# Performance work log

Measured on AMD Instinct MI355X. Metric: run time of the kernel, lower is better.

## Reference

```python
import jax, jax.numpy as jnp
import numpy as np

B, S, D, H, HD = 2, 2048, 1024, 16, 64
K, L = 1024, 4  # num_codes, vq_levels


def setup_inputs() -> dict:
    key = jax.random.key(0)
    ks = jax.random.split(key, 12)
    w = lambda k, shape: jax.random.normal(k, shape, jnp.float32) * 0.02
    return {
        "x": jax.random.normal(ks[0], (B, S, D), jnp.float32),
        "ln1_g": jnp.ones((D,), jnp.float32), "ln1_b": jnp.zeros((D,), jnp.float32),
        "wq": w(ks[1], (D, D)), "wk": w(ks[2], (D, D)), "wv": w(ks[3], (D, D)),
        "wg": w(ks[4], (D, D)), "wo": w(ks[5], (D, D)),
        "ln2_g": jnp.ones((D,), jnp.float32), "ln2_b": jnp.zeros((D,), jnp.float32),
        "w1": w(ks[6], (D, 4 * D)), "b1": jnp.zeros((4 * D,), jnp.float32),
        "w2": w(ks[7], (4 * D, D)), "b2": jnp.zeros((D,), jnp.float32),
        "ln3_g": jnp.ones((D,), jnp.float32), "ln3_b": jnp.zeros((D,), jnp.float32),
        "codebooks": jax.random.uniform(ks[8], (L, K, D), jnp.float32, -1.0 / K, 1.0 / K),
    }


def _ln(x, g, b):
    m = jnp.mean(x, -1, keepdims=True)
    v = jnp.var(x, -1, keepdims=True)
    return (x - m) / jnp.sqrt(v + 1e-5) * g + b


def _rope(x):  # x: [B, S, H, HD]
    hd = x.shape[-1]
    inv = 1.0 / (10000.0 ** (jnp.arange(0, hd, 2, dtype=jnp.float32) / hd))
    t = jnp.arange(x.shape[1], dtype=jnp.float32)
    f = jnp.einsum('i,j->ij', t, inv)               # [S, HD/2]
    emb = jnp.concatenate([f, f], -1)               # [S, HD]
    cos = jnp.cos(emb)[None, :, None, :]
    sin = jnp.sin(emb)[None, :, None, :]
    x1, x2 = jnp.split(x, 2, -1)
    rot = jnp.concatenate([-x2, x1], -1)
    return x * cos + rot * sin


def reference(x, ln1_g, ln1_b, wq, wk, wv, wg, wo, ln2_g, ln2_b,
              w1, b1, w2, b2, ln3_g, ln3_b, codebooks):
    # --- retention sub-block (pre-LN) ---
    h = _ln(x, ln1_g, ln1_b)
    q = (h @ wq).reshape(B, S, H, HD)
    k = (h @ wk).reshape(B, S, H, HD)
    v = (h @ wv).reshape(B, S, H, HD)
    q, k = _rope(q), _rope(k)
    q, k, v = (a.transpose(0, 2, 1, 3) for a in (q, k, v))  # [B,H,S,HD]
    i = jnp.arange(S)
    dmask = jnp.tril(i[:, None] - i[None, :]).astype(jnp.float32)  # [S,S], >=0
    gamma = (1.0 - jnp.exp2(-5.0 - jnp.arange(H, dtype=jnp.float32)))[:, None, None]
    decay = (gamma ** dmask) * jnp.tril(jnp.ones((S, S), jnp.float32))  # [H,S,S]
    ret = jnp.einsum('bhqd,bhkd->bhqk', q, k) / np.sqrt(HD).astype(np.float32) * decay
    o = jnp.einsum('bhqk,bhkd->bhqd', ret, v).transpose(0, 2, 1, 3).reshape(B, S, D)
    g = jax.nn.silu(h @ wg)
    x = x + (o * g) @ wo
    # --- MLP sub-block (pre-LN) ---
    h2 = _ln(x, ln2_g, ln2_b)
    x = x + (jax.nn.gelu(h2 @ w1 + b1, approximate=False) @ w2 + b2)
    # --- residual vector quantizer ---
    xn = _ln(x, ln3_g, ln3_b)
    residual, total = xn, jnp.zeros_like(xn)
    ql, el = 0.0, 0.0
    for lvl in range(L):
        cb = codebooks[lvl]                         # [K, D]
        flat = residual.reshape(-1, D)              # [B*S, D]
        d2 = (jnp.sum(flat ** 2, 1, keepdims=True)
              + jnp.sum(cb ** 2, 1) - 2.0 * flat @ cb.T)
        idx = jnp.argmin(d2, 1)
        quant = cb[idx].reshape(xn.shape)
        ql = ql + jnp.mean((quant - jax.lax.stop_gradient(residual)) ** 2)
        el = el + jnp.mean((jax.lax.stop_gradient(quant) - residual) ** 2)
        total = total + quant
        residual = residual - jax.lax.stop_gradient(quant)
    final = xn + jax.lax.stop_gradient(total - xn)  # straight-through
    return (x + final, ql / L, el / L)
```

## Files before the change

kernel.cpp:

```cpp
#include <hip/hip_runtime.h>
#include <cstdint>
#include <cstddef>

#define DEV __device__ __forceinline__

typedef __attribute__((ext_vector_type(8))) short bf16x8;
typedef __attribute__((ext_vector_type(4))) float f32x4;

typedef const __attribute__((address_space(1))) void gl_void;
typedef __attribute__((address_space(3))) void lds_void;

DEV unsigned short f2bf(float f){
  union { float f; uint32_t u; } v; v.f = f;
  uint32_t r = v.u + 0x7FFFu + ((v.u >> 16) & 1u);
  return (unsigned short)(r >> 16);
}
DEV float bf2f(unsigned short u){
  union { uint32_t u; float f; } v; v.u = ((uint32_t)u) << 16; return v.f;
}
DEV uint32_t packbf2(float a, float b){
  return (uint32_t)f2bf(a) | ((uint32_t)f2bf(b) << 16);
}

__global__ void ln_kernel(const float* __restrict__ x, const float* __restrict__ gw,
                          const float* __restrict__ bw, unsigned short* __restrict__ obf,
                          float* __restrict__ of32)
{
  const int row = blockIdx.x, t = threadIdx.x;
  const float4 v = ((const float4*)(x + (size_t)row*1024))[t];
  float s  = v.x + v.y + v.z + v.w;
  float s2 = v.x*v.x + v.y*v.y + v.z*v.z + v.w*v.w;
  #pragma unroll
  for (int o = 32; o >= 1; o >>= 1){ s += __shfl_down(s, o); s2 += __shfl_down(s2, o); }
  __shared__ float red[8];
  const int w = t >> 6, ln = t & 63;
  if (ln == 0){ red[w] = s; red[4+w] = s2; }
  __syncthreads();
  const float fs  = red[0]+red[1]+red[2]+red[3];
  const float fs2 = red[4]+red[5]+red[6]+red[7];
  const float mean = fs * (1.0f/1024.0f);
  const float var  = fs2 * (1.0f/1024.0f) - mean*mean;
  const float rstd = rsqrtf(var + 1e-5f);
  const float4 gv = ((const float4*)gw)[t];
  const float4 bv = ((const float4*)bw)[t];
  float4 o4;
  o4.x = (v.x-mean)*rstd*gv.x + bv.x;
  o4.y = (v.y-mean)*rstd*gv.y + bv.y;
  o4.z = (v.z-mean)*rstd*gv.z + bv.z;
  o4.w = (v.w-mean)*rstd*gv.w + bv.w;
  if (of32) ((float4*)(of32 + (size_t)row*1024))[t] = o4;
  ushort4 ob; ob.x = f2bf(o4.x); ob.y = f2bf(o4.y); ob.z = f2bf(o4.z); ob.w = f2bf(o4.w);
  ((ushort4*)(obf + (size_t)row*1024))[t] = ob;
}

struct Ptr5 { const float* p[5]; };
__global__ void transpose_cvt5(Ptr5 in, unsigned short* __restrict__ out)
{
  __shared__ float tile[32][33];
  const float* src = in.p[blockIdx.z];
  unsigned short* dst = out + (size_t)blockIdx.z*1048576;
  const int c0 = blockIdx.x*32, r0 = blockIdx.y*32;
  const int tx = threadIdx.x & 31, ty = threadIdx.x >> 5;
  #pragma unroll
  for (int i = 0; i < 32; i += 8)
    tile[ty+i][tx] = src[(size_t)(r0+ty+i)*1024 + c0 + tx];
  __syncthreads();
  #pragma unroll
  for (int i = 0; i < 32; i += 8)
    dst[(size_t)(c0+ty+i)*1024 + r0 + tx] = f2bf(tile[tx][ty+i]);
}

__global__ void transpose_cvt(const float* __restrict__ in, unsigned short* __restrict__ out,
                              int R, int C)
{
  __shared__ float tile[32][33];
  const int c0 = blockIdx.x*32, r0 = blockIdx.y*32;
  const int tx = threadIdx.x & 31, ty = threadIdx.x >> 5;
  #pragma unroll
  for (int i = 0; i < 32; i += 8)
    tile[ty+i][tx] = in[(size_t)(r0+ty+i)*C + c0 + tx];
  __syncthreads();
  #pragma unroll
  for (int i = 0; i < 32; i += 8)
    out[(size_t)(c0+ty+i)*R + r0 + tx] = f2bf(tile[tx][ty+i]);
}

__global__ void cvtnorm_kernel(const float* __restrict__ cb, unsigned short* __restrict__ cbbf,
                               float* __restrict__ cbn2)
{
  const int code = blockIdx.x, t = threadIdx.x;
  const float4 v = ((const float4*)(cb + (size_t)code*1024))[t];
  ushort4 o; o.x = f2bf(v.x); o.y = f2bf(v.y); o.z = f2bf(v.z); o.w = f2bf(v.w);
  ((ushort4*)(cbbf + (size_t)code*1024))[t] = o;
  float s = v.x*v.x + v.y*v.y + v.z*v.z + v.w*v.w;
  #pragma unroll
  for (int off = 32; off >= 1; off >>= 1) s += __shfl_down(s, off);
  __shared__ float red[4];
  if ((t & 63) == 0) red[t >> 6] = s;
  __syncthreads();
  if (t == 0) cbn2[code] = red[0]+red[1]+red[2]+red[3];
}

__global__ void rope_tab(float2* __restrict__ rt)
{
  const int i = blockIdx.x*256 + threadIdx.x;
  const int s = i >> 5, j = i & 31;
  const float ang = (float)s * exp2f(-(float)j * 0.4152410118609203f);
  float sn, cs; sincosf(ang, &sn, &cs);
  rt[i] = make_float2(cs, sn);
}

template<int EPI>
__global__ __launch_bounds__(512, 2) void gemm256(
    const unsigned short* __restrict__ A, const unsigned short* __restrict__ BT,
    unsigned short* __restrict__ C, const float* __restrict__ bias,
    const float2* __restrict__ rt, int M, int N, int K)
{
  __shared__ __align__(16) unsigned short SH[49152];
  const int t = threadIdx.x;
  const int w = t >> 6, ln = t & 63, lg = ln >> 4, lc = ln & 15;
  const int wm = w >> 2, wn = w & 3;
  const int gx = gridDim.x, nwg = gridDim.x * gridDim.y;
  int lin = blockIdx.y * gx + blockIdx.x;
  lin = (lin >> 3) + (lin & 7) * (nwg >> 3);
  const int m0 = (lin / gx) * 256, n0 = (lin % gx) * 256;
  const int nkt = K >> 5;

  f32x4 acc[8][4] = {};

  auto stage = [&](int buf, int kt){
    #pragma unroll
    for (int isB = 0; isB < 2; ++isB){
      const unsigned short* src = isB ? BT : A;
      const int mb = isB ? n0 : m0;
      #pragma unroll
      for (int j = 0; j < 2; ++j){
        const int u = j*512 + t;
        const int ro = u >> 2;
        const int su = (u & 3) ^ ((ro >> 1) & 3);
        __builtin_amdgcn_global_load_lds(
          (gl_void*)(src + (size_t)(mb + ro)*K + (size_t)kt*32 + su*8),
          (lds_void*)&SH[buf*16384 + isB*8192 + (j*512 + (t & ~63))*8],
          16, 0, 0);
      }
    }
  };

  auto ldA = [&](int buf, int mf) -> bf16x8 {
    const int R = wm*128 + mf*16 + lc;
    const int cu = lg ^ ((R >> 1) & 3);
    return *(const bf16x8*)&SH[buf*16384 + (R*4 + cu)*8];
  };
  auto ldB = [&](int buf, int nf) -> bf16x8 {
    const int R = wn*64 + nf*16 + lc;
    const int cu = lg ^ ((R >> 1) & 3);
    return *(const bf16x8*)&SH[buf*16384 + 8192 + (R*4 + cu)*8];
  };

  stage(0, 0); stage(1, 1);
  asm volatile("s_waitcnt vmcnt(4)" ::: "memory");
  __builtin_amdgcn_s_barrier();

  for (int kt = 0; kt < nkt; ++kt){
    const int cur = kt % 3;
    const bool pf = (kt + 2 < nkt);
    bf16x8 aF[4], bF[4];

    if (pf) stage((kt + 2) % 3, kt + 2);
    #pragma unroll
    for (int f = 0; f < 4; ++f){ aF[f] = ldA(cur, f); bF[f] = ldB(cur, f); }
    __builtin_amdgcn_s_barrier();
    __builtin_amdgcn_s_setprio(1);
    #pragma unroll
    for (int mf = 0; mf < 4; ++mf)
      #pragma unroll
      for (int nf = 0; nf < 4; ++nf)
        acc[mf][nf] = __builtin_amdgcn_mfma_f32_16x16x32_bf16(aF[mf], bF[nf], acc[mf][nf], 0, 0, 0);
    __builtin_amdgcn_s_setprio(0);
    asm volatile("s_waitcnt lgkmcnt(0)" ::: "memory");
    __builtin_amdgcn_s_barrier();

    #pragma unroll
    for (int f = 0; f < 4; ++f) aF[f] = ldA(cur, 4 + f);
    __builtin_amdgcn_s_barrier();
    __builtin_amdgcn_s_setprio(1);
    #pragma unroll
    for (int mf = 0; mf < 4; ++mf)
      #pragma unroll
      for (int nf = 0; nf < 4; ++nf)
        acc[4+mf][nf] = __builtin_amdgcn_mfma_f32_16x16x32_bf16(aF[mf], bF[nf], acc[4+mf][nf], 0, 0, 0);
    __builtin_amdgcn_s_setprio(0);
    asm volatile("s_waitcnt lgkmcnt(0)" ::: "memory");
    if (pf) asm volatile("s_waitcnt vmcnt(4)" ::: "memory");
    else    asm volatile("s_waitcnt vmcnt(0)" ::: "memory");
    __builtin_amdgcn_s_barrier();
  }

  const int mrow = m0 + wm*128, ncol = n0 + wn*64;
  if constexpr (EPI == 3){
    const int sect = ncol >> 10;
    unsigned short* outp = C + (size_t)sect*4194304;
    #pragma unroll
    for (int mf = 0; mf < 8; ++mf){
      #pragma unroll
      for (int r = 0; r < 4; ++r){
        const int row = mrow + mf*16 + lg*4 + r;
        const int s_ = row & 2047;
        #pragma unroll
        for (int nf = 0; nf < 4; ++nf){
          const int c1 = (ncol + nf*16 + lc) & 1023;
          float v = acc[mf][nf][r];
          if (sect <= 1){
            const float2 cs = rt[(s_ << 5) + (c1 & 31)];
            const float vp = acc[mf][nf ^ 2][r];
            v = (c1 & 32) ? (v*cs.x + vp*cs.y) : (v*cs.x - vp*cs.y);
          } else if (sect == 3){
            v = v * (1.0f / (1.0f + __expf(-v)));
          }
          outp[(size_t)row*1024 + c1] = f2bf(v);
        }
      }
    }
  } else {
    #pragma unroll
    for (int mf = 0; mf < 8; ++mf){
      #pragma unroll
      for (int r = 0; r < 4; ++r){
        const int row = mrow + mf*16 + lg*4 + r;
        #pragma unroll
        for (int nf = 0; nf < 4; ++nf){
          const int col = ncol + nf*16 + lc;
          float v = acc[mf][nf][r] + bias[col];
          v = 0.5f * v * (1.0f + erff(v * 0.70710678118654752f));
          C[(size_t)row*N + col] = f2bf(v);
        }
      }
    }
  }
}

template<int EPI, bool BIAS, bool RES, bool OUTBF, int NSPLIT>
__global__ __launch_bounds__(256, 2) void gemm64_bt(
    const unsigned short* __restrict__ A, const unsigned short* __restrict__ BT,
    void* __restrict__ Cv, const float* __restrict__ bias, const float* __restrict__ resid,
    int M, int N, int K)
{
  __shared__ __align__(16) unsigned short As[3][64*64];
  __shared__ __align__(16) unsigned short Bs[3][128*64];
  const int t = threadIdx.x;
  const int w = t >> 6, ln = t & 63, lg = ln >> 4, lc = ln & 15;
  const int gx = gridDim.x, nwg = gridDim.x * gridDim.y;
  int lin = blockIdx.y * gx + blockIdx.x;
  lin = (lin >> 3) + (lin & 7) * (nwg >> 3);
  const int bx = lin % gx, by = lin / gx;
  const int m0 = by * 64, n0 = bx * 128;
  const int wr = (w >> 1) * 32, wc = (w & 1) * 64;
  f32x4 acc[2][4] = {};
  const int nkt = (K >> 6) / NSPLIT;
  const int ktb = (NSPLIT > 1) ? blockIdx.z * nkt : 0;

  auto stage = [&](int buf, int kt){
    #pragma unroll
    for (int c = 0; c < 2; ++c){
      const int chunk = c*256 + t;
      const int row = chunk >> 3;
      const int kb = (((chunk & 7) << 4) ^ ((row & 7) << 4)) >> 1;
      __builtin_amdgcn_global_load_lds(
          (gl_void*)(A + (size_t)(m0+row)*K + (size_t)(ktb+kt)*64 + kb),
          (lds_void*)&As[buf][(c*256 + w*64)*8], 16, 0, 0);
    }
    #pragma unroll
    for (int c = 0; c < 4; ++c){
      const int chunk = c*256 + t;
      const int row = chunk >> 3;
      const int kb = (((chunk & 7) << 4) ^ ((row & 7) << 4)) >> 1;
      __builtin_amdgcn_global_load_lds(
          (gl_void*)(BT + (size_t)(n0+row)*K + (size_t)(ktb+kt)*64 + kb),
          (lds_void*)&Bs[buf][(c*256 + w*64)*8], 16, 0, 0);
    }
  };

  stage(0, 0); stage(1, 1);
  asm volatile("s_waitcnt vmcnt(6)" ::: "memory");
  __builtin_amdgcn_s_barrier();

  for (int kt = 0; kt < nkt; ++kt){
    const int cur = kt % 3;
    const bool pf = (kt + 2 < nkt);
    if (pf) stage((kt + 2) % 3, kt + 2);
    __builtin_amdgcn_s_setprio(1);
    #pragma unroll
    for (int ks = 0; ks < 2; ++ks){
      bf16x8 af[2], bfr[4];
      #pragma unroll
      for (int i = 0; i < 2; ++i){
        const int rowA = wr + i*16 + lc;
        const int colA = (((ks<<6) + (lg<<4)) ^ ((rowA & 7) << 4)) >> 1;
        af[i] = *(const bf16x8*)&As[cur][rowA*64 + colA];
      }
      #pragma unroll
      for (int i = 0; i < 4; ++i){
        const int rowB = wc + i*16 + lc;
        const int colB = (((ks<<6) + (lg<<4)) ^ ((rowB & 7) << 4)) >> 1;
        bfr[i] = *(const bf16x8*)&Bs[cur][rowB*64 + colB];
      }
      #pragma unroll
      for (int m = 0; m < 2; ++m)
        #pragma unroll
        for (int n = 0; n < 4; ++n)
          acc[m][n] = __builtin_amdgcn_mfma_f32_16x16x32_bf16(af[m], bfr[n], acc[m][n], 0, 0, 0);
    }
    __builtin_amdgcn_s_setprio(0);
    asm volatile("s_waitcnt lgkmcnt(0)" ::: "memory");
    if (pf) asm volatile("s_waitcnt vmcnt(6)" ::: "memory");
    else    asm volatile("s_waitcnt vmcnt(0)" ::: "memory");
    __builtin_amdgcn_s_barrier();
  }

  if constexpr (EPI == 4){
    #pragma unroll
    for (int m = 0; m < 2; ++m){
      #pragma unroll
      for (int r = 0; r < 4; ++r){
        float best = 3.4e38f; int bi = 0;
        #pragma unroll
        for (int n = 0; n < 4; ++n){
          const int col = n0 + wc + n*16 + lc;
          const float d = bias[col] - 2.0f*acc[m][n][r];
          if (d < best){ best = d; bi = col; }
        }
        #pragma unroll
        for (int o = 1; o < 16; o <<= 1){
          const float ob = __shfl_xor(best, o);
          const int oi = __shfl_xor(bi, o);
          if (ob < best || (ob == best && oi < bi)){ best = ob; bi = oi; }
        }
        if (lc == 0){
          const int row = m0 + wr + m*16 + lg*4 + r;
          ((float2*)Cv)[row*16 + bx*2 + (w & 1)] = make_float2(best, (float)bi);
        }
      }
    }
    return;
  }

  float* Cp = (float*)Cv + (NSPLIT > 1 ? (size_t)blockIdx.z * (size_t)M * N : 0);
  #pragma unroll
  for (int m = 0; m < 2; ++m){
    #pragma unroll
    for (int n = 0; n < 4; ++n){
      #pragma unroll
      for (int r = 0; r < 4; ++r){
        const int row = m0 + wr + m*16 + lg*4 + r;
        const int col = n0 + wc + n*16 + lc;
        float v = acc[m][n][r];
        if constexpr (BIAS) v += bias[col];
        if constexpr (RES) v += resid[(size_t)row*N + col];
        if constexpr (OUTBF) ((unsigned short*)Cv)[(size_t)row*N + col] = f2bf(v);
        else                 Cp[(size_t)row*N + col] = v;
      }
    }
  }
}

__global__ void splitk_reduce(const float* __restrict__ p, const float* __restrict__ bias,
                              const float* __restrict__ resid, float* __restrict__ out)
{
  const int i = blockIdx.x*256 + threadIdx.x;
  const float4 a = ((const float4*)p)[i];
  const float4 b = ((const float4*)(p + 4194304))[i];
  const float4 rv = ((const float4*)resid)[i];
  const float4 bv = ((const float4*)bias)[i & 255];
  float4 o;
  o.x = a.x + b.x + rv.x + bv.x;
  o.y = a.y + b.y + rv.y + bv.y;
  o.z = a.z + b.z + rv.z + bv.z;
  o.w = a.w + b.w + rv.w + bv.w;
  ((float4*)out)[i] = o;
}

__global__ __launch_bounds__(256, 2) void chunk_sum(
    const unsigned short* __restrict__ kb, const unsigned short* __restrict__ vb,
    float* __restrict__ Tbuf)
{
  __shared__ unsigned short KT[64*72];
  __shared__ unsigned short VT[64*72];
  const int t = threadIdx.x, w = t >> 6, ln = t & 63, lg = ln >> 4, lc = ln & 15;
  const int blk = blockIdx.x;
  const int bh = blk >> 5, c = blk & 31;
  const int b = bh >> 4, hh = bh & 15;
  const float lg2g = log2f(1.0f - exp2f(-5.0f - (float)hh));
  #pragma unroll
  for (int ch = 0; ch < 2; ++ch){
    const int chunk = ch*256 + t;
    const int i = chunk >> 3, d0 = (chunk & 7)*8;
    const size_t gofs = ((size_t)(b*2048 + c*64 + i))*1024 + hh*64 + d0;
    const float wi = exp2f(lg2g * (float)(64 - i));
    union {uint4 u; unsigned short s[8];} kv, vv;
    kv.u = *(const uint4*)(kb + gofs);
    vv.u = *(const uint4*)(vb + gofs);
    #pragma unroll
    for (int j = 0; j < 8; ++j){
      KT[(d0+j)*72 + i] = f2bf(bf2f(kv.s[j]) * wi);
      VT[(d0+j)*72 + i] = vv.s[j];
    }
  }
  __syncthreads();
  f32x4 acc[4] = {};
  #pragma unroll
  for (int ks = 0; ks < 2; ++ks){
    const bf16x8 af = *(const bf16x8*)&KT[(w*16 + lc)*72 + ks*32 + lg*8];
    #pragma unroll
    for (int n = 0; n < 4; ++n){
      const bf16x8 bf = *(const bf16x8*)&VT[(n*16 + lc)*72 + ks*32 + lg*8];
      acc[n] = __builtin_amdgcn_mfma_f32_16x16x32_bf16(af, bf, acc[n], 0, 0, 0);
    }
  }
  float* out = Tbuf + (size_t)blk*4096;
  #pragma unroll
  for (int n = 0; n < 4; ++n)
    #pragma unroll
    for (int r = 0; r < 4; ++r)
      out[(w*16 + lg*4 + r)*64 + n*16 + lc] = acc[n][r];
}

__global__ void chunk_scan(const float* __restrict__ Tbuf, unsigned short* __restrict__ statesT)
{
  const int bh = blockIdx.x, t = threadIdx.x;
  const int hh = bh & 15;
  const float gamma = 1.0f - exp2f(-5.0f - (float)hh);
  const float g64 = exp2f(log2f(gamma) * 64.0f);
  float S[16];
  #pragma unroll
  for (int j = 0; j < 16; ++j) S[j] = 0.f;
  const int dv = t >> 2, d0 = (t & 3) * 16;
  for (int c = 0; c < 32; ++c){
    const size_t base = ((size_t)(bh*32 + c))*4096;
    union { unsigned short s[8]; uint4 u; } p0, p1;
    #pragma unroll
    for (int j = 0; j < 8; ++j){ p0.s[j] = f2bf(S[j]); p1.s[j] = f2bf(S[8+j]); }
    *(uint4*)(statesT + base + t*16)     = p0.u;
    *(uint4*)(statesT + base + t*16 + 8) = p1.u;
    #pragma unroll
    for (int j = 0; j < 16; ++j)
      S[j] = g64*S[j] + Tbuf[base + (size_t)(d0 + j)*64 + dv];
  }
}

__global__ __launch_bounds__(256, 2) void retention_chunk(
    const unsigned short* __restrict__ qb, const unsigned short* __restrict__ kb,
    const unsigned short* __restrict__ vb, const unsigned short* __restrict__ gb,
    const unsigned short* __restrict__ statesT, unsigned short* __restrict__ og)
{
  __shared__ unsigned short VT[64*72];
  __shared__ unsigned short Pw[64*72];
  const int t = threadIdx.x, w = t >> 6, ln = t & 63, lg = ln >> 4, lc = ln & 15;
  const int blk = blockIdx.x;
  const int bh = blk >> 5, c = blk & 31;
  const int b = bh >> 4, hh = bh & 15;
  const float lg2g = log2f(1.0f - exp2f(-5.0f - (float)hh));
  float gpr[4];
  #pragma unroll
  for (int r = 0; r < 4; ++r) gpr[r] = exp2f(-lg2g * (float)r);
  const size_t rowbase = (size_t)(b*2048 + c*64);

  #pragma unroll
  for (int ch = 0; ch < 2; ++ch){
    const int chunk = ch*256 + t;
    const int i = chunk >> 3, d0 = (chunk & 7)*8;
    union {uint4 u; unsigned short s[8];} vv;
    vv.u = *(const uint4*)(vb + (rowbase + i)*1024 + hh*64 + d0);
    #pragma unroll
    for (int j = 0; j < 8; ++j) VT[(d0+j)*72 + i] = vv.s[j];
  }

  bf16x8 Qf[2], Kf[4][2];
  #pragma unroll
  for (int ks = 0; ks < 2; ++ks){
    union {uint4 u; bf16x8 f;} cv;
    cv.u = *(const uint4*)(qb + (rowbase + w*16 + lc)*1024 + hh*64 + ks*32 + lg*8);
    Qf[ks] = cv.f;
    #pragma unroll
    for (int mt = 0; mt < 4; ++mt){
      union {uint4 u; bf16x8 f;} kv;
      kv.u = *(const uint4*)(kb + (rowbase + mt*16 + lc)*1024 + hh*64 + ks*32 + lg*8);
      Kf[mt][ks] = kv.f;
    }
  }

  f32x4 st[4] = {};
  #pragma unroll
  for (int ks = 0; ks < 2; ++ks)
    #pragma unroll
    for (int mt = 0; mt < 4; ++mt)
      st[mt] = __builtin_amdgcn_mfma_f32_16x16x32_bf16(Kf[mt][ks], Qf[ks], st[mt], 0, 0, 0);

  __syncthreads();

  #pragma unroll
  for (int mt = 0; mt < 4; ++mt){
    const int kp = mt*16 + lg*4;
    const int qrow = w*16 + lc;
    const int delta0 = qrow - kp;
    const float dec0 = exp2f(lg2g * (float)delta0) * 0.125f;
    float vals[4];
    #pragma unroll
    for (int r = 0; r < 4; ++r)
      vals[r] = (delta0 >= r) ? st[mt][r] * dec0 * gpr[r] : 0.0f;
    uint2 pk; pk.x = packbf2(vals[0], vals[1]); pk.y = packbf2(vals[2], vals[3]);
    *(uint2*)&Pw[qrow*72 + kp] = pk;
  }

  f32x4 acc[4] = {};
  const unsigned short* Sbase = statesT + (size_t)blk*4096;
  #pragma unroll
  for (int ks = 0; ks < 2; ++ks)
    #pragma unroll
    for (int n = 0; n < 4; ++n){
      union {uint4 u; bf16x8 f;} sv;
      sv.u = *(const uint4*)(Sbase + (n*16 + lc)*64 + ks*32 + lg*8);
      acc[n] = __builtin_amdgcn_mfma_f32_16x16x32_bf16(Qf[ks], sv.f, acc[n], 0, 0, 0);
    }
  #pragma unroll
  for (int n = 0; n < 4; ++n)
    #pragma unroll
    for (int r = 0; r < 4; ++r)
      acc[n][r] *= exp2f(lg2g * (float)(w*16 + lg*4 + r)) * 0.125f;

  #pragma unroll
  for (int ks = 0; ks < 2; ++ks){
    const bf16x8 Pf = *(const bf16x8*)&Pw[(w*16 + lc)*72 + ks*32 + lg*8];
    #pragma unroll
    for (int n = 0; n < 4; ++n){
      const bf16x8 Vf = *(const bf16x8*)&VT[(n*16 + lc)*72 + ks*32 + lg*8];
      acc[n] = __builtin_amdgcn_mfma_f32_16x16x32_bf16(Pf, Vf, acc[n], 0, 0, 0);
    }
  }

  #pragma unroll
  for (int n = 0; n < 4; ++n){
    #pragma unroll
    for (int r = 0; r < 4; ++r){
      const size_t row = rowbase + w*16 + lg*4 + r;
      const int col = hh*64 + n*16 + lc;
      const float gv = bf2f(gb[row*1024 + col]);
      og[row*1024 + col] = f2bf(acc[n][r] * gv);
    }
  }
}

__global__ void rvq_update3(const float* __restrict__ cb_l, const float2* __restrict__ partials,
                            const float* __restrict__ res_in, float* __restrict__ res_out,
                            unsigned short* __restrict__ resb, float* __restrict__ qlpart, int lvl)
{
  const int m = blockIdx.x, t = threadIdx.x;
  __shared__ int sid;
  if (t == 0){
    float best = 3.4e38f; int bi = 0;
    #pragma unroll
    for (int p = 0; p < 16; ++p){
      const float2 pr = partials[m*16 + p];
      if (pr.x < best){ best = pr.x; bi = (int)pr.y; }
    }
    sid = bi;
  }
  __syncthreads();
  const int id = sid;
  const float4 qv = ((const float4*)(cb_l + (size_t)id*1024))[t];
  const float4 rv = ((const float4*)(res_in + (size_t)m*1024))[t];
  float4 nr; nr.x = rv.x - qv.x; nr.y = rv.y - qv.y; nr.z = rv.z - qv.z; nr.w = rv.w - qv.w;
  ((float4*)(res_out + (size_t)m*1024))[t] = nr;
  ushort4 nb; nb.x = f2bf(nr.x); nb.y = f2bf(nr.y); nb.z = f2bf(nr.z); nb.w = f2bf(nr.w);
  ((ushort4*)(resb + (size_t)m*1024))[t] = nb;
  float s = nr.x*nr.x + nr.y*nr.y + nr.z*nr.z + nr.w*nr.w;
  #pragma unroll
  for (int o = 32; o >= 1; o >>= 1) s += __shfl_down(s, o);
  __shared__ float red[4];
  if ((t & 63) == 0) red[t >> 6] = s;
  __syncthreads();
  if (t == 0) qlpart[lvl*4096 + m] = red[0]+red[1]+red[2]+red[3];
}

__global__ void final_add3(const float* __restrict__ x2, const float* __restrict__ xn,
                           const float* __restrict__ res4, float* __restrict__ out)
{
  const int i = blockIdx.x*256 + threadIdx.x;
  const float4 a = ((const float4*)x2)[i];
  const float4 b = ((const float4*)xn)[i];
  const float4 c = ((const float4*)res4)[i];
  float4 o;
  o.x = a.x + b.x - c.x;
  o.y = a.y + b.y - c.y;
  o.z = a.z + b.z - c.z;
  o.w = a.w + b.w - c.w;
  ((float4*)out)[i] = o;
}

__global__ void ql_final(const float* __restrict__ qlpart, float* __restrict__ outs)
{
  const int t = threadIdx.x;
  float s = 0.f;
  for (int i = t; i < 16384; i += 256) s += qlpart[i];
  #pragma unroll
  for (int o = 32; o >= 1; o >>= 1) s += __shfl_down(s, o);
  __shared__ float red[4];
  if ((t & 63) == 0) red[t >> 6] = s;
  __syncthreads();
  if (t == 0){
    const float q = (red[0]+red[1]+red[2]+red[3]) * (1.0f/4194304.0f) * 0.25f;
    outs[0] = q; outs[1] = q;
  }
}

extern "C" void kernel_launch(void* const* d_in, const int* in_sizes, int n_in,
                              void* d_out, int out_size, void* d_ws, size_t ws_size,
                              hipStream_t stream)
{
  const float* x     = (const float*)d_in[0];
  const float* ln1_g = (const float*)d_in[1];
  const float* ln1_b = (const float*)d_in[2];
  const float* wq    = (const float*)d_in[3];
  const float* wk    = (const float*)d_in[4];
  const float* wv    = (const float*)d_in[5];
  const float* wg    = (const float*)d_in[6];
  const float* wo    = (const float*)d_in[7];
  const float* ln2_g = (const float*)d_in[8];
  const float* ln2_b = (const float*)d_in[9];
  const float* w1    = (const float*)d_in[10];
  const float* b1    = (const float*)d_in[11];
  const float* w2    = (const float*)d_in[12];
  const float* b2    = (const float*)d_in[13];
  const float* ln3_g = (const float*)d_in[14];
  const float* ln3_b = (const float*)d_in[15];
  const float* cb    = (const float*)d_in[16];

  char* ws = (char*)d_ws;
  const size_t MB = 1024*1024;
  unsigned short* wqkvgT = (unsigned short*)(ws + 0*MB);
  unsigned short* w1T  = (unsigned short*)(ws + 10*MB);
  unsigned short* w2T  = (unsigned short*)(ws + 18*MB);
  unsigned short* cbbf = (unsigned short*)(ws + 26*MB);
  float* cbn2     = (float*)(ws + 34*MB);
  float* qlpart   = (float*)(ws + 34*MB + 16*1024);
  float2* partials= (float2*)(ws + 34*MB + 128*1024);
  unsigned short* hbf  = (unsigned short*)(ws + 35*MB);
  unsigned short* qbuf = (unsigned short*)(ws + 43*MB);
  unsigned short* kbuf = (unsigned short*)(ws + 51*MB);
  unsigned short* vbuf = (unsigned short*)(ws + 59*MB);
  unsigned short* gbuf = (unsigned short*)(ws + 67*MB);
  float* skbuf  = (float*)(ws + 43*MB);
  unsigned short* ogb  = (unsigned short*)(ws + 75*MB);
  float* x1     = (float*)(ws + 83*MB);
  unsigned short* h2   = (unsigned short*)(ws + 99*MB);
  unsigned short* a1   = (unsigned short*)(ws + 107*MB);
  float* x2     = (float*)(ws + 139*MB);
  float* Tbuf   = (float*)(ws + 139*MB);
  float* xnf    = (float*)(ws + 155*MB);
  unsigned short* statesT = (unsigned short*)(ws + 155*MB);
  unsigned short* resb = (unsigned short*)(ws + 171*MB);
  float2* rtab  = (float2*)(ws + 179*MB);
  float* resw   = (float*)(ws + 187*MB);

  float* outf = (float*)d_out;

  Ptr5 p5; p5.p[0]=wq; p5.p[1]=wk; p5.p[2]=wv; p5.p[3]=wg; p5.p[4]=wo;
  hipLaunchKernelGGL(transpose_cvt5, dim3(32,32,5), dim3(256), 0, stream, p5, wqkvgT);
  hipLaunchKernelGGL(transpose_cvt, dim3(128,32), dim3(256), 0, stream, w1, w1T, 1024, 4096);
  hipLaunchKernelGGL(transpose_cvt, dim3(32,128), dim3(256), 0, stream, w2, w2T, 4096, 1024);
  hipLaunchKernelGGL(cvtnorm_kernel, dim3(4096), dim3(256), 0, stream, cb, cbbf, cbn2);
  hipLaunchKernelGGL(rope_tab, dim3(256), dim3(256), 0, stream, rtab);

  hipLaunchKernelGGL(ln_kernel, dim3(4096), dim3(256), 0, stream, x, ln1_g, ln1_b, hbf, (float*)nullptr);
  hipLaunchKernelGGL((gemm256<3>), dim3(16,16), dim3(512), 0, stream,
                     hbf, wqkvgT, qbuf, (const float*)nullptr, (const float2*)rtab, 4096, 4096, 1024);
  hipLaunchKernelGGL(chunk_sum,  dim3(1024), dim3(256), 0, stream, kbuf, vbuf, Tbuf);
  hipLaunchKernelGGL(chunk_scan, dim3(32),   dim3(256), 0, stream, Tbuf, statesT);
  hipLaunchKernelGGL(retention_chunk, dim3(1024), dim3(256), 0, stream,
                     qbuf, kbuf, vbuf, gbuf, statesT, ogb);
  hipLaunchKernelGGL((gemm64_bt<0,false,true,false,1>), dim3(8,64), dim3(256), 0, stream,
                     ogb, wqkvgT + 4194304, (void*)x1, (const float*)nullptr, x, 4096, 1024, 1024);

  hipLaunchKernelGGL(ln_kernel, dim3(4096), dim3(256), 0, stream, x1, ln2_g, ln2_b, h2, (float*)nullptr);
  hipLaunchKernelGGL((gemm256<2>), dim3(16,16), dim3(512), 0, stream,
                     h2, w1T, a1, b1, (const float2*)rtab, 4096, 4096, 1024);
  hipLaunchKernelGGL((gemm64_bt<0,false,false,false,2>), dim3(8,64,2), dim3(256), 0, stream,
                     a1, w2T, (void*)skbuf, (const float*)nullptr, (const float*)nullptr, 4096, 1024, 4096);
  hipLaunchKernelGGL(splitk_reduce, dim3(4096), dim3(256), 0, stream, skbuf, b2, x1, x2);

  hipLaunchKernelGGL(ln_kernel, dim3(4096), dim3(256), 0, stream, x2, ln3_g, ln3_b, resb, xnf);
  for (int lvl = 0; lvl < 4; ++lvl){
    hipLaunchKernelGGL((gemm64_bt<4,false,false,false,1>), dim3(8,64), dim3(256), 0, stream,
                       resb, cbbf + (size_t)lvl*1048576, (void*)partials,
                       cbn2 + lvl*1024, (const float*)nullptr, 4096, 1024, 1024);
    hipLaunchKernelGGL(rvq_update3, dim3(4096), dim3(256), 0, stream,
                       cb + (size_t)lvl*1048576, partials,
                       (lvl == 0) ? xnf : resw, resw, resb, qlpart, lvl);
  }

  hipLaunchKernelGGL(final_add3, dim3(4096), dim3(256), 0, stream, x2, xnf, resw, outf);
  hipLaunchKernelGGL(ql_final, dim3(1), dim3(256), 0, stream, qlpart, outf + 4194304);
}
```

Baseline: 446.4 us.

## Stage GEMM epilogue through LDS, parallelize chunk scan, fuse final RVQ add

The gemm256 epilogue now writes each 16-row fragment into a per-wave LDS scratch and stores it to global memory as 16-byte vectors, replacing scattered 2-byte stores. The chunk_scan kernel is split over four times as many blocks, each thread carrying four state elements instead of sixteen. The last RVQ update level also computes the final output sum directly, removing the separate final_add3 kernel and one full residual write and read. The LDS staging reuses the SH buffer after the main loop and assumes it is no longer needed there.

Measured after the change: 426.8 us. 4.4% less time.

```diff
diff --git a/kernel.cpp b/kernel.cpp
--- a/kernel.cpp
+++ b/kernel.cpp
@@ -196,10 +196,13 @@
     __builtin_amdgcn_s_barrier();
   }
 
+  unsigned short* wls = &SH[w*1024];
   const int mrow = m0 + wm*128, ncol = n0 + wn*64;
+  const int rr0 = ln >> 3, cc0 = (ln & 7)*8;
   if constexpr (EPI == 3){
     const int sect = ncol >> 10;
     unsigned short* outp = C + (size_t)sect*4194304;
+    const int cbase = ncol & 1023;
     #pragma unroll
     for (int mf = 0; mf < 8; ++mf){
       #pragma unroll
@@ -208,7 +211,7 @@
         const int s_ = row & 2047;
         #pragma unroll
         for (int nf = 0; nf < 4; ++nf){
-          const int c1 = (ncol + nf*16 + lc) & 1023;
+          const int c1 = cbase + nf*16 + lc;
           float v = acc[mf][nf][r];
           if (sect <= 1){
             const float2 cs = rt[(s_ << 5) + (c1 & 31)];
@@ -217,23 +220,34 @@
           } else if (sect == 3){
             v = v * (1.0f / (1.0f + __expf(-v)));
           }
-          outp[(size_t)row*1024 + c1] = f2bf(v);
+          wls[(lg*4+r)*64 + nf*16 + lc] = f2bf(v);
         }
       }
+      #pragma unroll
+      for (int i = 0; i < 2; ++i){
+        const int rr = rr0 + 8*i;
+        const bf16x8 vv = *(const bf16x8*)&wls[rr*64 + cc0];
+        *(bf16x8*)(outp + (size_t)(mrow + mf*16 + rr)*1024 + cbase + cc0) = vv;
+      }
     }
   } else {
     #pragma unroll
     for (int mf = 0; mf < 8; ++mf){
       #pragma unroll
       for (int r = 0; r < 4; ++r){
-        const int row = mrow + mf*16 + lg*4 + r;
         #pragma unroll
         for (int nf = 0; nf < 4; ++nf){
           const int col = ncol + nf*16 + lc;
           float v = acc[mf][nf][r] + bias[col];
           v = 0.5f * v * (1.0f + erff(v * 0.70710678118654752f));
-          C[(size_t)row*N + col] = f2bf(v);
+          wls[(lg*4+r)*64 + nf*16 + lc] = f2bf(v);
         }
+      }
+      #pragma unroll
+      for (int i = 0; i < 2; ++i){
+        const int rr = rr0 + 8*i;
+        const bf16x8 vv = *(const bf16x8*)&wls[rr*64 + cc0];
+        *(bf16x8*)(C + (size_t)(mrow + mf*16 + rr)*N + ncol + cc0) = vv;
       }
     }
   }
@@ -426,24 +440,20 @@
 
 __global__ void chunk_scan(const float* __restrict__ Tbuf, unsigned short* __restrict__ statesT)
 {
-  const int bh = blockIdx.x, t = threadIdx.x;
+  const int bh = blockIdx.x, q = blockIdx.y, t = threadIdx.x;
   const int hh = bh & 15;
   const float gamma = 1.0f - exp2f(-5.0f - (float)hh);
   const float g64 = exp2f(log2f(gamma) * 64.0f);
-  float S[16];
-  #pragma unroll
-  for (int j = 0; j < 16; ++j) S[j] = 0.f;
-  const int dv = t >> 2, d0 = (t & 3) * 16;
+  float S[4] = {0.f, 0.f, 0.f, 0.f};
+  const int dv = t >> 2;
+  const int j0 = q*16 + (t & 3)*4;
   for (int c = 0; c < 32; ++c){
     const size_t base = ((size_t)(bh*32 + c))*4096;
-    union { unsigned short s[8]; uint4 u; } p0, p1;
-    #pragma unroll
-    for (int j = 0; j < 8; ++j){ p0.s[j] = f2bf(S[j]); p1.s[j] = f2bf(S[8+j]); }
-    *(uint4*)(statesT + base + t*16)     = p0.u;
-    *(uint4*)(statesT + base + t*16 + 8) = p1.u;
-    #pragma unroll
-    for (int j = 0; j < 16; ++j)
-      S[j] = g64*S[j] + Tbuf[base + (size_t)(d0 + j)*64 + dv];
+    ushort4 p; p.x = f2bf(S[0]); p.y = f2bf(S[1]); p.z = f2bf(S[2]); p.w = f2bf(S[3]);
+    *(ushort4*)(statesT + base + dv*64 + j0) = p;
+    #pragma unroll
+    for (int j = 0; j < 4; ++j)
+      S[j] = g64*S[j] + Tbuf[base + (size_t)(j0 + j)*64 + dv];
   }
 }
 
@@ -549,9 +559,12 @@
   }
 }
 
+template<int FINAL>
 __global__ void rvq_update3(const float* __restrict__ cb_l, const float2* __restrict__ partials,
                             const float* __restrict__ res_in, float* __restrict__ res_out,
-                            unsigned short* __restrict__ resb, float* __restrict__ qlpart, int lvl)
+                            unsigned short* __restrict__ resb, float* __restrict__ qlpart, int lvl,
+                            const float* __restrict__ x2, const float* __restrict__ xn,
+                            float* __restrict__ outf)
 {
   const int m = blockIdx.x, t = threadIdx.x;
   __shared__ int sid;
@@ -569,9 +582,20 @@
   const float4 qv = ((const float4*)(cb_l + (size_t)id*1024))[t];
   const float4 rv = ((const float4*)(res_in + (size_t)m*1024))[t];
   float4 nr; nr.x = rv.x - qv.x; nr.y = rv.y - qv.y; nr.z = rv.z - qv.z; nr.w = rv.w - qv.w;
-  ((float4*)(res_out + (size_t)m*1024))[t] = nr;
-  ushort4 nb; nb.x = f2bf(nr.x); nb.y = f2bf(nr.y); nb.z = f2bf(nr.z); nb.w = f2bf(nr.w);
-  ((ushort4*)(resb + (size_t)m*1024))[t] = nb;
+  if constexpr (FINAL){
+    const float4 a = ((const float4*)(x2 + (size_t)m*1024))[t];
+    const float4 b = ((const float4*)(xn + (size_t)m*1024))[t];
+    float4 o;
+    o.x = a.x + b.x - nr.x;
+    o.y = a.y + b.y - nr.y;
+    o.z = a.z + b.z - nr.z;
+    o.w = a.w + b.w - nr.w;
+    ((float4*)(outf + (size_t)m*1024))[t] = o;
+  } else {
+    ((float4*)(res_out + (size_t)m*1024))[t] = nr;
+    ushort4 nb; nb.x = f2bf(nr.x); nb.y = f2bf(nr.y); nb.z = f2bf(nr.z); nb.w = f2bf(nr.w);
+    ((ushort4*)(resb + (size_t)m*1024))[t] = nb;
+  }
   float s = nr.x*nr.x + nr.y*nr.y + nr.z*nr.z + nr.w*nr.w;
   #pragma unroll
   for (int o = 32; o >= 1; o >>= 1) s += __shfl_down(s, o);
@@ -579,21 +603,6 @@
   if ((t & 63) == 0) red[t >> 6] = s;
   __syncthreads();
   if (t == 0) qlpart[lvl*4096 + m] = red[0]+red[1]+red[2]+red[3];
-}
-
-__global__ void final_add3(const float* __restrict__ x2, const float* __restrict__ xn,
-                           const float* __restrict__ res4, float* __restrict__ out)
-{
-  const int i = blockIdx.x*256 + threadIdx.x;
-  const float4 a = ((const float4*)x2)[i];
-  const float4 b = ((const float4*)xn)[i];
-  const float4 c = ((const float4*)res4)[i];
-  float4 o;
-  o.x = a.x + b.x - c.x;
-  o.y = a.y + b.y - c.y;
-  o.z = a.z + b.z - c.z;
-  o.w = a.w + b.w - c.w;
-  ((float4*)out)[i] = o;
 }
 
 __global__ void ql_final(const float* __restrict__ qlpart, float* __restrict__ outs)
@@ -674,7 +683,7 @@
   hipLaunchKernelGGL((gemm256<3>), dim3(16,16), dim3(512), 0, stream,
                      hbf, wqkvgT, qbuf, (const float*)nullptr, (const float2*)rtab, 4096, 4096, 1024);
   hipLaunchKernelGGL(chunk_sum,  dim3(1024), dim3(256), 0, stream, kbuf, vbuf, Tbuf);
-  hipLaunchKernelGGL(chunk_scan, dim3(32),   dim3(256), 0, stream, Tbuf, statesT);
+  hipLaunchKernelGGL(chunk_scan, dim3(32,4), dim3(256), 0, stream, Tbuf, statesT);
   hipLaunchKernelGGL(retention_chunk, dim3(1024), dim3(256), 0, stream,
                      qbuf, kbuf, vbuf, gbuf, statesT, ogb);
   hipLaunchKernelGGL((gemm64_bt<0,false,true,false,1>), dim3(8,64), dim3(256), 0, stream,
@@ -692,11 +701,17 @@
     hipLaunchKernelGGL((gemm64_bt<4,false,false,false,1>), dim3(8,64), dim3(256), 0, stream,
                        resb, cbbf + (size_t)lvl*1048576, (void*)partials,
                        cbn2 + lvl*1024, (const float*)nullptr, 4096, 1024, 1024);
-    hipLaunchKernelGGL(rvq_update3, dim3(4096), dim3(256), 0, stream,
-                       cb + (size_t)lvl*1048576, partials,
-                       (lvl == 0) ? xnf : resw, resw, resb, qlpart, lvl);
-  }
-
-  hipLaunchKernelGGL(final_add3, dim3(4096), dim3(256), 0, stream, x2, xnf, resw, outf);
+    if (lvl < 3)
+      hipLaunchKernelGGL((rvq_update3<0>), dim3(4096), dim3(256), 0, stream,
+                         cb + (size_t)lvl*1048576, partials,
+                         (lvl == 0) ? xnf : resw, resw, resb, qlpart, lvl,
+                         (const float*)nullptr, (const float*)nullptr, (float*)nullptr);
+    else
+      hipLaunchKernelGGL((rvq_update3<1>), dim3(4096), dim3(256), 0, stream,
+                         cb + (size_t)lvl*1048576, partials,
+                         resw, (float*)nullptr, (unsigned short*)nullptr, qlpart, lvl,
+                         x2, xnf, outf);
+  }
+
   hipLaunchKernelGGL(ql_final, dim3(1), dim3(256), 0, stream, qlpart, outf + 4194304);
 }
```
